# Performance work log

Hardware: AMD Instinct MI355X
Metric: run time of the kernel (lower is better)

## Reference

```python
import jax, jax.numpy as jnp
import numpy as np

N_NODES = 100000
N_EDGES = 3200000
IN_DIM, HID_DIM, OUT_DIM = 384, 128, 5


def gcn_conv(x, src, dst, W, b, num_nodes):
    # PyG GCNConv: add self-loops, symmetric normalization, linear, aggregate, bias
    h = x @ W  # [N, out]
    ones = jnp.ones(src.shape[0], dtype=h.dtype)
    deg = jax.ops.segment_sum(ones, dst, num_segments=num_nodes)  # includes self-loops
    dinv = jnp.where(deg > 0, jax.lax.rsqrt(deg), 0.0)
    norm = dinv[src] * dinv[dst]  # [E+N]
    msg = h[src] * norm[:, None]
    out = jax.ops.segment_sum(msg, dst, num_segments=num_nodes)
    return out + b


def setup_inputs() -> dict:
    key = jax.random.key(0)
    ks = jax.random.split(key, 8)
    x = jax.random.normal(ks[0], (N_NODES, IN_DIM), dtype=jnp.float32)
    edge_index = jax.random.randint(ks[1], (2, N_EDGES), 0, N_NODES, dtype=jnp.int64)
    # Glorot-ish init for GCN linear weights
    def glorot(k, fi, fo):
        s = jnp.sqrt(6.0 / (fi + fo))
        return jax.random.uniform(k, (fi, fo), jnp.float32, -s, s)
    W1 = glorot(ks[2], IN_DIM, HID_DIM)
    b1 = jnp.zeros((HID_DIM,), jnp.float32)
    W2 = glorot(ks[3], HID_DIM, HID_DIM)
    b2 = jnp.zeros((HID_DIM,), jnp.float32)
    W3 = glorot(ks[4], HID_DIM, OUT_DIM)
    b3 = jnp.zeros((OUT_DIM,), jnp.float32)
    return {"x": x, "edge_index": edge_index, "W1": W1, "b1": b1,
            "W2": W2, "b2": b2, "W3": W3, "b3": b3}


def reference(x, edge_index, W1, b1, W2, b2, W3, b3):
    num_nodes = x.shape[0]
    loops = jnp.arange(num_nodes, dtype=edge_index.dtype)
    src = jnp.concatenate([edge_index[0], loops])
    dst = jnp.concatenate([edge_index[1], loops])
    # layer 1: GCNConv + ReLU (dropout is identity at inference)
    h = jax.nn.relu(gcn_conv(x, src, dst, W1, b1, num_nodes))
    # layer 2
    h = jax.nn.relu(gcn_conv(h, src, dst, W2, b2, num_nodes))
    # final layer: logits, no activation
    return gcn_conv(h, src, dst, W3, b3, num_nodes)
```

## Files before the change

kernel.cpp:

```cpp
#include <hip/hip_runtime.h>

#define NN 100000
#define NE 3200000
#define SCAN_CHUNK 1024

#define BSH 8
#define BKT_NODES 256
#define NBKT ((NN + BKT_NODES - 1) / BKT_NODES)
#define BIN_BLOCKS 256
#define EPB ((NE + BIN_BLOCKS - 1) / BIN_BLOCKS)
#define GH (NBKT * BIN_BLOCKS)

typedef unsigned int uint;
typedef unsigned short ushort;
typedef __attribute__((ext_vector_type(8))) short short8;
typedef __attribute__((ext_vector_type(4))) float f32x4;

__device__ inline void gload16(const void* g, void* l) {
    __builtin_amdgcn_global_load_lds(
        (const __attribute__((address_space(1))) void*)g,
        (__attribute__((address_space(3))) void*)l, 16, 0, 0);
}

__device__ inline ushort bf16rne(float x) {
    uint u = __float_as_uint(x);
    u += 0x7FFFu + ((u >> 16) & 1u);
    return (ushort)(u >> 16);
}
__device__ inline void split2(float x, ushort& h, ushort& l) {
    h = bf16rne(x);
    float hf = __uint_as_float((uint)h << 16);
    l = bf16rne(x - hf);
}
__device__ inline uint bf16pair(float a, float b) {
    uint ua = __float_as_uint(a);
    uint ub = __float_as_uint(b);
    ua += 0x7FFFu + ((ua >> 16) & 1u);
    ub += 0x7FFFu + ((ub >> 16) & 1u);
    return (ua >> 16) | (ub & 0xFFFF0000u);
}
__device__ inline float bflo(uint u) { return __uint_as_float(u << 16); }
__device__ inline float bfhi(uint u) { return __uint_as_float(u & 0xFFFF0000u); }

__global__ __launch_bounds__(256) void hist_bkt(const int* __restrict__ dst,
                                                int* __restrict__ ghist) {
    __shared__ int h[NBKT];
    int t = threadIdx.x;
    for (int i = t; i < NBKT; i += 256) h[i] = 0;
    __syncthreads();
    int beg = blockIdx.x * EPB;
    int end = beg + EPB; if (end > NE) end = NE;
    for (int e = beg + t; e < end; e += 256)
        atomicAdd(&h[dst[e] >> BSH], 1);
    __syncthreads();
    for (int i = t; i < NBKT; i += 256)
        ghist[i * BIN_BLOCKS + blockIdx.x] = h[i];
}

__global__ __launch_bounds__(256) void scan_p1(const int* __restrict__ cnt,
                                               int* __restrict__ bsum, int N) {
    int t = threadIdx.x;
    int base = blockIdx.x * SCAN_CHUNK + t * 4;
    int s = 0;
#pragma unroll
    for (int q = 0; q < 4; q++) {
        int i = base + q;
        if (i < N) s += cnt[i];
    }
    __shared__ int red[4];
#pragma unroll
    for (int off = 32; off; off >>= 1) s += __shfl_down(s, off, 64);
    if ((t & 63) == 0) red[t >> 6] = s;
    __syncthreads();
    if (t == 0) bsum[blockIdx.x] = red[0] + red[1] + red[2] + red[3];
}

__global__ void scan_p2(int* __restrict__ bsum, int nb) {
    __shared__ int s[128];
    int t = threadIdx.x;
    int v = (t < nb) ? bsum[t] : 0;
    s[t] = v;
    __syncthreads();
    for (int off = 1; off < 128; off <<= 1) {
        int x = s[t];
        int add = (t >= off) ? s[t - off] : 0;
        __syncthreads();
        s[t] = x + add;
        __syncthreads();
    }
    if (t < nb) bsum[t] = s[t] - v;
}

__global__ __launch_bounds__(256) void scan_p3_plain(int* __restrict__ data,
                                                     const int* __restrict__ bsum, int N) {
    __shared__ int ts[256];
    int t = threadIdx.x;
    int base = blockIdx.x * SCAN_CHUNK + t * 4;
    int c[4];
    int s = 0;
#pragma unroll
    for (int q = 0; q < 4; q++) {
        int i = base + q;
        c[q] = (i < N) ? data[i] : 0;
        s += c[q];
    }
    ts[t] = s;
    __syncthreads();
    for (int off = 1; off < 256; off <<= 1) {
        int x = ts[t];
        int add = (t >= off) ? ts[t - off] : 0;
        __syncthreads();
        ts[t] = x + add;
        __syncthreads();
    }
    int run = bsum[blockIdx.x] + ts[t] - s;
#pragma unroll
    for (int q = 0; q < 4; q++) {
        int i = base + q;
        if (i < N) { data[i] = run; run += c[q]; }
    }
}

__global__ __launch_bounds__(256) void scan_p3_deg(const int* __restrict__ cnt,
                                                   const int* __restrict__ bsum,
                                                   int* __restrict__ rowptr,
                                                   float* __restrict__ dinv, int N) {
    __shared__ int ts[256];
    int t = threadIdx.x;
    int base = blockIdx.x * SCAN_CHUNK + t * 4;
    int c[4];
    int s = 0;
#pragma unroll
    for (int q = 0; q < 4; q++) {
        int i = base + q;
        c[q] = (i < N) ? cnt[i] : 0;
        s += c[q];
    }
    ts[t] = s;
    __syncthreads();
    for (int off = 1; off < 256; off <<= 1) {
        int x = ts[t];
        int add = (t >= off) ? ts[t - off] : 0;
        __syncthreads();
        ts[t] = x + add;
        __syncthreads();
    }
    int run = bsum[blockIdx.x] + ts[t] - s;
#pragma unroll
    for (int q = 0; q < 4; q++) {
        int i = base + q;
        if (i < N) {
            rowptr[i] = run;
            dinv[i] = 1.0f / sqrtf((float)(c[q] + 1));
            run += c[q];
        }
    }
    if (base < N && N <= base + 4) rowptr[N] = run;
}

__global__ __launch_bounds__(256) void bin_edges(const int* __restrict__ src,
                                                 const int* __restrict__ dst,
                                                 const int* __restrict__ ghist,
                                                 uint* __restrict__ binned) {
    __shared__ int cur[NBKT];
    int t = threadIdx.x;
    for (int i = t; i < NBKT; i += 256) cur[i] = ghist[i * BIN_BLOCKS + blockIdx.x];
    __syncthreads();
    int beg = blockIdx.x * EPB;
    int end = beg + EPB; if (end > NE) end = NE;
    for (int e = beg + t; e < end; e += 256) {
        int d = dst[e];
        int b = d >> BSH;
        int p = atomicAdd(&cur[b], 1);
        binned[p] = ((uint)src[e] << BSH) | (uint)(d & (BKT_NODES - 1));
    }
}

__global__ __launch_bounds__(256) void bucket_count(const uint* __restrict__ binned,
                                                    const int* __restrict__ ghist,
                                                    int* __restrict__ cnt) {
    __shared__ int c[BKT_NODES];
    int t = threadIdx.x;
    int bkt = blockIdx.x;
    for (int i = t; i < BKT_NODES; i += 256) c[i] = 0;
    __syncthreads();
    int beg = ghist[bkt * BIN_BLOCKS];
    int end = (bkt == NBKT - 1) ? NE : ghist[(bkt + 1) * BIN_BLOCKS];
    for (int j = beg + t; j < end; j += 256)
        atomicAdd(&c[binned[j] & (BKT_NODES - 1)], 1);
    __syncthreads();
    int base = bkt * BKT_NODES;
    int nb = NN - base; if (nb > BKT_NODES) nb = BKT_NODES;
    for (int i = t; i < nb; i += 256) cnt[base + i] = c[i];
}

__global__ __launch_bounds__(256) void csr_fill(const uint* __restrict__ binned,
                                                const int* __restrict__ ghist,
                                                const int* __restrict__ rowptr,
                                                int* __restrict__ col) {
    __shared__ int fill[BKT_NODES];
    int t = threadIdx.x;
    int bkt = blockIdx.x;
    for (int i = t; i < BKT_NODES; i += 256) fill[i] = 0;
    __syncthreads();
    int beg = ghist[bkt * BIN_BLOCKS];
    int end = (bkt == NBKT - 1) ? NE : ghist[(bkt + 1) * BIN_BLOCKS];
    int base = bkt * BKT_NODES;
    for (int j = beg + t; j < end; j += 256) {
        uint r = binned[j];
        int dl = r & (BKT_NODES - 1);
        int p = rowptr[base + dl] + atomicAdd(&fill[dl], 1);
        col[p] = (int)(r >> BSH);
    }
}

template <int K>
__global__ __launch_bounds__(256) void wsplit(const float* __restrict__ W,
                                              ushort* __restrict__ Wth,
                                              ushort* __restrict__ Wtl) {
    __shared__ float tile[32][128];
    int t = threadIdx.x;
    int kb = blockIdx.x;
    {
        int k = t >> 3, cq = t & 7;
#pragma unroll
        for (int q = 0; q < 4; q++) {
            float4 v = *(const float4*)&W[(size_t)(kb * 32 + k) * 128 + cq * 16 + q * 4];
            *(float4*)&tile[k][cq * 16 + q * 4] = v;
        }
    }
    __syncthreads();
    {
        int c = t >> 1, g = t & 1;
        ushort hs[16], ls[16];
#pragma unroll
        for (int i = 0; i < 16; i++) split2(tile[g * 16 + i][c], hs[i], ls[i]);
        uint h[8], lo[8];
#pragma unroll
        for (int i = 0; i < 8; i++) {
            h[i] = (uint)hs[2 * i] | ((uint)hs[2 * i + 1] << 16);
            lo[i] = (uint)ls[2 * i] | ((uint)ls[2 * i + 1] << 16);
        }
        size_t o = (size_t)c * K + kb * 32 + g * 16;
        *(uint4*)&Wth[o] = make_uint4(h[0], h[1], h[2], h[3]);
        *(uint4*)&Wth[o + 8] = make_uint4(h[4], h[5], h[6], h[7]);
        *(uint4*)&Wtl[o] = make_uint4(lo[0], lo[1], lo[2], lo[3]);
        *(uint4*)&Wtl[o + 8] = make_uint4(lo[4], lo[5], lo[6], lo[7]);
    }
}

template <int K>
__global__ __launch_bounds__(256) void mfma_gemm(const float* __restrict__ X,
                                                 const ushort* __restrict__ Wth,
                                                 const ushort* __restrict__ Wtl,
                                                 const float* __restrict__ dinv,
                                                 uint* __restrict__ Y, int M) {
    __shared__ char smem[32 * 1024];
    char* aHi = smem;
    char* aLo = smem + 8192;
    char* bHi = smem + 16384;
    char* bLo = smem + 24576;
    int tid = threadIdx.x;
    int w = tid >> 6, l = tid & 63;
    int rowBase = blockIdx.x * 128;

    f32x4 acc[2][8];
#pragma unroll
    for (int mf = 0; mf < 2; mf++)
#pragma unroll
        for (int n = 0; n < 8; n++) acc[mf][n] = (f32x4){0.f, 0.f, 0.f, 0.f};

    int sRow = tid >> 1, sKp = tid & 1;
    int gRow = rowBase + sRow;
    bool rowOK = gRow < M;
    size_t aBase = (size_t)(rowOK ? gRow : 0) * K + sKp * 16;

    float4 a0, a1, a2, a3;
    a0 = a1 = a2 = a3 = make_float4(0.f, 0.f, 0.f, 0.f);
    if (rowOK) {
        a0 = *(const float4*)&X[aBase];
        a1 = *(const float4*)&X[aBase + 4];
        a2 = *(const float4*)&X[aBase + 8];
        a3 = *(const float4*)&X[aBase + 12];
    }

    int fc = l & 15, fkg = l >> 4;

    for (int kt = 0; kt < K; kt += 32) {
#pragma unroll
        for (int i = 0; i < 2; i++) {
            int cb = (i * 4 + w) * 64;
            int c = cb + l;
            int colb = c >> 2, kg = c & 3;
            size_t go = (size_t)colb * K + kt + kg * 8;
            gload16(&Wth[go], bHi + cb * 16);
            gload16(&Wtl[go], bLo + cb * 16);
        }
        {
            float v[16] = {a0.x, a0.y, a0.z, a0.w, a1.x, a1.y, a1.z, a1.w,
                           a2.x, a2.y, a2.z, a2.w, a3.x, a3.y, a3.z, a3.w};
            uint hh[8], hl[8];
#pragma unroll
            for (int i = 0; i < 8; i++) {
                ushort h0, l0, h1, l1;
                split2(v[2 * i], h0, l0);
                split2(v[2 * i + 1], h1, l1);
                hh[i] = (uint)h0 | ((uint)h1 << 16);
                hl[i] = (uint)l0 | ((uint)l1 << 16);
            }
            int wa = (sRow * 4 + sKp * 2) * 16;
            *(uint4*)(aHi + wa) = make_uint4(hh[0], hh[1], hh[2], hh[3]);
            *(uint4*)(aHi + wa + 16) = make_uint4(hh[4], hh[5], hh[6], hh[7]);
            *(uint4*)(aLo + wa) = make_uint4(hl[0], hl[1], hl[2], hl[3]);
            *(uint4*)(aLo + wa + 16) = make_uint4(hl[4], hl[5], hl[6], hl[7]);
        }
        __syncthreads();

        if (kt + 32 < K && rowOK) {
            size_t nb = aBase + kt + 32;
            a0 = *(const float4*)&X[nb];
            a1 = *(const float4*)&X[nb + 4];
            a2 = *(const float4*)&X[nb + 8];
            a3 = *(const float4*)&X[nb + 12];
        }

#pragma unroll
        for (int mf = 0; mf < 2; mf++) {
            int aoff = (((2 * w + mf) * 16 + fc) * 4 + fkg) * 16;
            short8 ah = *(const short8*)(aHi + aoff);
            short8 al = *(const short8*)(aLo + aoff);
#pragma unroll
            for (int n = 0; n < 8; n++) {
                int boff = ((16 * n + fc) * 4 + fkg) * 16;
                short8 bh = *(const short8*)(bHi + boff);
                short8 bl = *(const short8*)(bLo + boff);
                acc[mf][n] = __builtin_amdgcn_mfma_f32_16x16x32_bf16(ah, bh, acc[mf][n], 0, 0, 0);
                acc[mf][n] = __builtin_amdgcn_mfma_f32_16x16x32_bf16(ah, bl, acc[mf][n], 0, 0, 0);
                acc[mf][n] = __builtin_amdgcn_mfma_f32_16x16x32_bf16(al, bh, acc[mf][n], 0, 0, 0);
            }
        }
        __syncthreads();
    }

#pragma unroll
    for (int mf = 0; mf < 2; mf++) {
        float dscale[4];
#pragma unroll
        for (int r = 0; r < 4; r++) {
            int row = rowBase + (2 * w + mf) * 16 + fkg * 4 + r;
            dscale[r] = (row < M) ? dinv[row] : 0.f;
        }
#pragma unroll
        for (int n = 0; n < 8; n++) {
#pragma unroll
            for (int r = 0; r < 4; r++) {
                float val = acc[mf][n][r] * dscale[r];
                float p = __shfl_xor(val, 1, 64);
                int row = rowBase + (2 * w + mf) * 16 + fkg * 4 + r;
                if (!(l & 1) && row < M)
                    Y[(size_t)row * 64 + 8 * n + (fc >> 1)] = bf16pair(val, p);
            }
        }
    }
}

__global__ void gemm_n5(const float* __restrict__ X, const float* __restrict__ W,
                        float* __restrict__ Y, int M) {
    int idx = blockIdx.x * 256 + threadIdx.x;
    int row = idx / 5, c = idx % 5;
    if (row >= M) return;
    float acc = 0.f;
#pragma unroll 8
    for (int k = 0; k < 128; k++) acc += X[row * 128 + k] * W[k * 5 + c];
    Y[row * 5 + c] = acc;
}

__global__ void pack5(const float* __restrict__ Y, const float* __restrict__ dinv,
                      uint4* __restrict__ hc, int N) {
    int node = blockIdx.x * 256 + threadIdx.x;
    if (node >= N) return;
    float di = dinv[node];
    float v0 = Y[node * 5 + 0] * di;
    float v1 = Y[node * 5 + 1] * di;
    float v2 = Y[node * 5 + 2] * di;
    float v3 = Y[node * 5 + 3] * di;
    float v4 = Y[node * 5 + 4] * di;
    hc[node] = make_uint4(bf16pair(v0, v1), bf16pair(v2, v3), bf16pair(v4, 0.f), 0u);
}

#define ACC8(v)                         \
    a0 += bflo(v.x); a1 += bfhi(v.x);   \
    a2 += bflo(v.y); a3 += bfhi(v.y);   \
    a4 += bflo(v.z); a5 += bfhi(v.z);   \
    a6 += bflo(v.w); a7 += bfhi(v.w);

__global__ __launch_bounds__(256) void agg128_v3(const uint4* __restrict__ hb4,
                                                 const int* __restrict__ rowptr,
                                                 const int* __restrict__ col,
                                                 const float* __restrict__ dinv,
                                                 const float* __restrict__ bias,
                                                 float* __restrict__ out, int N, int do_relu) {
    int wave = threadIdx.x >> 6;
    int lane = threadIdx.x & 63;
    int node = blockIdx.x * 4 + wave;
    if (node >= N) return;
    int g = lane >> 4;
    int q = lane & 15;
    int beg = rowptr[node], end = rowptr[node + 1];
    float a0 = 0.f, a1 = 0.f, a2 = 0.f, a3 = 0.f, a4 = 0.f, a5 = 0.f, a6 = 0.f, a7 = 0.f;

    int j = beg;
    for (; j + 16 <= end; j += 16) {
        int s0 = col[j + g];
        int s1 = col[j + 4 + g];
        int s2 = col[j + 8 + g];
        int s3 = col[j + 12 + g];
        uint4 v0 = hb4[(size_t)s0 * 16 + q];
        uint4 v1 = hb4[(size_t)s1 * 16 + q];
        uint4 v2 = hb4[(size_t)s2 * 16 + q];
        uint4 v3 = hb4[(size_t)s3 * 16 + q];
        ACC8(v0); ACC8(v1); ACC8(v2); ACC8(v3);
    }
    if (j + 8 <= end) {
        int s0 = col[j + g];
        int s1 = col[j + 4 + g];
        uint4 v0 = hb4[(size_t)s0 * 16 + q];
        uint4 v1 = hb4[(size_t)s1 * 16 + q];
        ACC8(v0); ACC8(v1);
        j += 8;
    }
    if (j < end) {
        int jj0 = j + g, jj1 = j + 4 + g;
        bool p0 = jj0 < end, p1 = jj1 < end;
        int s0 = p0 ? col[jj0] : node;
        int s1 = p1 ? col[jj1] : node;
        uint4 v0 = hb4[(size_t)s0 * 16 + q];
        uint4 v1 = hb4[(size_t)s1 * 16 + q];
        if (!p0) v0 = make_uint4(0u, 0u, 0u, 0u);
        if (!p1) v1 = make_uint4(0u, 0u, 0u, 0u);
        ACC8(v0); ACC8(v1);
    }
#pragma unroll
    for (int off = 16; off <= 32; off <<= 1) {
        a0 += __shfl_xor(a0, off, 64);
        a1 += __shfl_xor(a1, off, 64);
        a2 += __shfl_xor(a2, off, 64);
        a3 += __shfl_xor(a3, off, 64);
        a4 += __shfl_xor(a4, off, 64);
        a5 += __shfl_xor(a5, off, 64);
        a6 += __shfl_xor(a6, off, 64);
        a7 += __shfl_xor(a7, off, 64);
    }
    if (g == 0) {
        uint4 vs = hb4[(size_t)node * 16 + q];
        ACC8(vs);
        float di = dinv[node];
        const float4* bias4 = (const float4*)bias;
        float4 bb0 = bias4[q * 2], bb1 = bias4[q * 2 + 1];
        float o0 = a0 * di + bb0.x, o1 = a1 * di + bb0.y;
        float o2 = a2 * di + bb0.z, o3 = a3 * di + bb0.w;
        float o4 = a4 * di + bb1.x, o5 = a5 * di + bb1.y;
        float o6 = a6 * di + bb1.z, o7 = a7 * di + bb1.w;
        if (do_relu) {
            o0 = fmaxf(o0, 0.f); o1 = fmaxf(o1, 0.f);
            o2 = fmaxf(o2, 0.f); o3 = fmaxf(o3, 0.f);
            o4 = fmaxf(o4, 0.f); o5 = fmaxf(o5, 0.f);
            o6 = fmaxf(o6, 0.f); o7 = fmaxf(o7, 0.f);
        }
        float4* out4 = (float4*)out;
        out4[(size_t)node * 32 + q * 2] = make_float4(o0, o1, o2, o3);
        out4[(size_t)node * 32 + q * 2 + 1] = make_float4(o4, o5, o6, o7);
    }
}

__global__ void agg5_v2(const uint4* __restrict__ hc, const int* __restrict__ rowptr,
                        const int* __restrict__ col, const float* __restrict__ dinv,
                        const float* __restrict__ b3, float* __restrict__ out, int N) {
    int node = blockIdx.x * 256 + threadIdx.x;
    if (node >= N) return;
    float a0 = 0.f, a1 = 0.f, a2 = 0.f, a3 = 0.f, a4 = 0.f;
    int beg = rowptr[node], end = rowptr[node + 1];
#pragma unroll 2
    for (int j = beg; j < end; ++j) {
        uint4 v = hc[col[j]];
        a0 += bflo(v.x); a1 += bfhi(v.x);
        a2 += bflo(v.y); a3 += bfhi(v.y);
        a4 += bflo(v.z);
    }
    uint4 vs = hc[node];
    a0 += bflo(vs.x); a1 += bfhi(vs.x);
    a2 += bflo(vs.y); a3 += bfhi(vs.y);
    a4 += bflo(vs.z);
    float di = dinv[node];
    out[node * 5 + 0] = a0 * di + b3[0];
    out[node * 5 + 1] = a1 * di + b3[1];
    out[node * 5 + 2] = a2 * di + b3[2];
    out[node * 5 + 3] = a3 * di + b3[3];
    out[node * 5 + 4] = a4 * di + b3[4];
}

static inline size_t align512(size_t x) { return (x + 511) & ~(size_t)511; }

extern "C" void kernel_launch(void* const* d_in, const int* in_sizes, int n_in,
                              void* d_out, int out_size, void* d_ws, size_t ws_size,
                              hipStream_t stream) {
    const float* x  = (const float*)d_in[0];
    const int* ei   = (const int*)d_in[1];
    const float* W1 = (const float*)d_in[2];
    const float* b1 = (const float*)d_in[3];
    const float* W2 = (const float*)d_in[4];
    const float* b2 = (const float*)d_in[5];
    const float* W3 = (const float*)d_in[6];
    const float* b3 = (const float*)d_in[7];
    const int* src = ei;
    const int* dst = ei + NE;

    char* ws = (char*)d_ws;
    size_t off = 0;
    int* cnt = (int*)(ws + off);        off += align512((size_t)NN * 4);
    int* rowptr = (int*)(ws + off);     off += align512((size_t)(NN + 1) * 4);
    float* dinv = (float*)(ws + off);   off += align512((size_t)NN * 4);
    int* bsum = (int*)(ws + off);       off += align512((size_t)128 * 4);
    int* ghist = (int*)(ws + off);      off += align512((size_t)GH * 4);
    ushort* wt1h = (ushort*)(ws + off); off += align512((size_t)128 * 384 * 2);
    ushort* wt1l = (ushort*)(ws + off); off += align512((size_t)128 * 384 * 2);
    ushort* wt2h = (ushort*)(ws + off); off += align512((size_t)128 * 128 * 2);
    ushort* wt2l = (ushort*)(ws + off); off += align512((size_t)128 * 128 * 2);
    int* col = (int*)(ws + off);        off += align512((size_t)NE * 4);
    uint* hb = (uint*)(ws + off);       off += align512((size_t)NN * 64 * 4);
    float* bufF = (float*)(ws + off);   off += align512((size_t)NN * 128 * 4);
    float* bufC = (float*)(ws + off);   off += align512((size_t)NN * 5 * 4);
    uint4* hc = (uint4*)(ws + off);     off += align512((size_t)NN * 16);
    uint* binned = (uint*)bufF;
    (void)ws_size;

    wsplit<384><<<12, 256, 0, stream>>>(W1, wt1h, wt1l);
    wsplit<128><<<4, 256, 0, stream>>>(W2, wt2h, wt2l);

    hist_bkt<<<BIN_BLOCKS, 256, 0, stream>>>(dst, ghist);
    {
        int nb = (GH + SCAN_CHUNK - 1) / SCAN_CHUNK;
        scan_p1<<<nb, 256, 0, stream>>>(ghist, bsum, GH);
        scan_p2<<<1, 128, 0, stream>>>(bsum, nb);
        scan_p3_plain<<<nb, 256, 0, stream>>>(ghist, bsum, GH);
    }
    bin_edges<<<BIN_BLOCKS, 256, 0, stream>>>(src, dst, ghist, binned);
    bucket_count<<<NBKT, 256, 0, stream>>>(binned, ghist, cnt);
    {
        int nb = (NN + SCAN_CHUNK - 1) / SCAN_CHUNK;
        scan_p1<<<nb, 256, 0, stream>>>(cnt, bsum, NN);
        scan_p2<<<1, 128, 0, stream>>>(bsum, nb);
        scan_p3_deg<<<nb, 256, 0, stream>>>(cnt, bsum, rowptr, dinv, NN);
    }
    csr_fill<<<NBKT, 256, 0, stream>>>(binned, ghist, rowptr, col);

    int gemm_blocks = (NN + 127) / 128;
    mfma_gemm<384><<<gemm_blocks, 256, 0, stream>>>(x, wt1h, wt1l, dinv, hb, NN);
    agg128_v3<<<(NN + 3) / 4, 256, 0, stream>>>((const uint4*)hb, rowptr, col, dinv, b1, bufF, NN, 1);
    mfma_gemm<128><<<gemm_blocks, 256, 0, stream>>>(bufF, wt2h, wt2l, dinv, hb, NN);
    agg128_v3<<<(NN + 3) / 4, 256, 0, stream>>>((const uint4*)hb, rowptr, col, dinv, b2, bufF, NN, 1);
    gemm_n5<<<((NN * 5) + 255) / 256, 256, 0, stream>>>(bufF, W3, bufC, NN);
    pack5<<<(NN + 255) / 256, 256, 0, stream>>>(bufC, dinv, hc, NN);
    agg5_v2<<<(NN + 255) / 256, 256, 0, stream>>>(hc, rowptr, col, dinv, b3, (float*)d_out, NN);
}
```

Measured before the change: 495.9 us.

## Switch GEMMs and intermediates from split bf16 to fp16 with fewer MFMAs

```diff
diff --git a/kernel.cpp b/kernel.cpp
--- a/kernel.cpp
+++ b/kernel.cpp
@@ -1,4 +1,5 @@
 #include <hip/hip_runtime.h>
+#include <hip/hip_fp16.h>
 
 #define NN 100000
 #define NE 3200000
@@ -13,7 +14,7 @@
 
 typedef unsigned int uint;
 typedef unsigned short ushort;
-typedef __attribute__((ext_vector_type(8))) short short8;
+typedef __attribute__((ext_vector_type(8))) _Float16 half8;
 typedef __attribute__((ext_vector_type(4))) float f32x4;
 
 __device__ inline void gload16(const void* g, void* l) {
@@ -22,25 +23,17 @@
         (__attribute__((address_space(3))) void*)l, 16, 0, 0);
 }
 
-__device__ inline ushort bf16rne(float x) {
-    uint u = __float_as_uint(x);
-    u += 0x7FFFu + ((u >> 16) & 1u);
-    return (ushort)(u >> 16);
-}
-__device__ inline void split2(float x, ushort& h, ushort& l) {
-    h = bf16rne(x);
-    float hf = __uint_as_float((uint)h << 16);
-    l = bf16rne(x - hf);
-}
-__device__ inline uint bf16pair(float a, float b) {
-    uint ua = __float_as_uint(a);
-    uint ub = __float_as_uint(b);
-    ua += 0x7FFFu + ((ua >> 16) & 1u);
-    ub += 0x7FFFu + ((ub >> 16) & 1u);
-    return (ua >> 16) | (ub & 0xFFFF0000u);
-}
-__device__ inline float bflo(uint u) { return __uint_as_float(u << 16); }
-__device__ inline float bfhi(uint u) { return __uint_as_float(u & 0xFFFF0000u); }
+__device__ inline uint f2h_pair(float a, float b) {
+    return (uint)__half_as_ushort(__float2half(a)) |
+           ((uint)__half_as_ushort(__float2half(b)) << 16);
+}
+__device__ inline float h2f_lo(uint u) { return __half2float(__ushort_as_half((ushort)(u & 0xFFFFu))); }
+__device__ inline float h2f_hi(uint u) { return __half2float(__ushort_as_half((ushort)(u >> 16))); }
+__device__ inline void splitH(float x, ushort& h, ushort& l) {
+    __half hh = __float2half(x);
+    h = __half_as_ushort(hh);
+    l = __half_as_ushort(__float2half(x - __half2float(hh)));
+}
 
 __global__ __launch_bounds__(256) void hist_bkt(const int* __restrict__ dst,
                                                 int* __restrict__ ghist) {
@@ -234,7 +227,7 @@
         int c = t >> 1, g = t & 1;
         ushort hs[16], ls[16];
 #pragma unroll
-        for (int i = 0; i < 16; i++) split2(tile[g * 16 + i][c], hs[i], ls[i]);
+        for (int i = 0; i < 16; i++) splitH(tile[g * 16 + i][c], hs[i], ls[i]);
         uint h[8], lo[8];
 #pragma unroll
         for (int i = 0; i < 8; i++) {
@@ -250,16 +243,15 @@
 }
 
 template <int K>
-__global__ __launch_bounds__(256) void mfma_gemm(const float* __restrict__ X,
-                                                 const ushort* __restrict__ Wth,
-                                                 const ushort* __restrict__ Wtl,
-                                                 const float* __restrict__ dinv,
-                                                 uint* __restrict__ Y, int M) {
-    __shared__ char smem[32 * 1024];
-    char* aHi = smem;
-    char* aLo = smem + 8192;
-    char* bHi = smem + 16384;
-    char* bLo = smem + 24576;
+__global__ __launch_bounds__(256) void mfma_gemm_f32(const float* __restrict__ X,
+                                                     const ushort* __restrict__ Wth,
+                                                     const ushort* __restrict__ Wtl,
+                                                     const float* __restrict__ dinv,
+                                                     uint* __restrict__ Y, int M) {
+    __shared__ char smem[24 * 1024];
+    char* aP = smem;
+    char* bH = smem + 8192;
+    char* bL = smem + 16384;
     int tid = threadIdx.x;
     int w = tid >> 6, l = tid & 63;
     int rowBase = blockIdx.x * 128;
@@ -285,34 +277,27 @@
     }
 
     int fc = l & 15, fkg = l >> 4;
+    int aoff0 = fkg * 2048 + ((2 * w + 0) * 16 + fc) * 16;
+    int aoff1 = fkg * 2048 + ((2 * w + 1) * 16 + fc) * 16;
 
     for (int kt = 0; kt < K; kt += 32) {
 #pragma unroll
         for (int i = 0; i < 2; i++) {
             int cb = (i * 4 + w) * 64;
             int c = cb + l;
-            int colb = c >> 2, kg = c & 3;
+            int kg = c >> 7, colb = c & 127;
             size_t go = (size_t)colb * K + kt + kg * 8;
-            gload16(&Wth[go], bHi + cb * 16);
-            gload16(&Wtl[go], bLo + cb * 16);
+            gload16(&Wth[go], bH + cb * 16);
+            gload16(&Wtl[go], bL + cb * 16);
         }
         {
             float v[16] = {a0.x, a0.y, a0.z, a0.w, a1.x, a1.y, a1.z, a1.w,
                            a2.x, a2.y, a2.z, a2.w, a3.x, a3.y, a3.z, a3.w};
-            uint hh[8], hl[8];
-#pragma unroll
-            for (int i = 0; i < 8; i++) {
-                ushort h0, l0, h1, l1;
-                split2(v[2 * i], h0, l0);
-                split2(v[2 * i + 1], h1, l1);
-                hh[i] = (uint)h0 | ((uint)h1 << 16);
-                hl[i] = (uint)l0 | ((uint)l1 << 16);
-            }
-            int wa = (sRow * 4 + sKp * 2) * 16;
-            *(uint4*)(aHi + wa) = make_uint4(hh[0], hh[1], hh[2], hh[3]);
-            *(uint4*)(aHi + wa + 16) = make_uint4(hh[4], hh[5], hh[6], hh[7]);
-            *(uint4*)(aLo + wa) = make_uint4(hl[0], hl[1], hl[2], hl[3]);
-            *(uint4*)(aLo + wa + 16) = make_uint4(hl[4], hl[5], hl[6], hl[7]);
+            uint hh[8];
+#pragma unroll
+            for (int i = 0; i < 8; i++) hh[i] = f2h_pair(v[2 * i], v[2 * i + 1]);
+            *(uint4*)(aP + (2 * sKp) * 2048 + sRow * 16) = make_uint4(hh[0], hh[1], hh[2], hh[3]);
+            *(uint4*)(aP + (2 * sKp + 1) * 2048 + sRow * 16) = make_uint4(hh[4], hh[5], hh[6], hh[7]);
         }
         __syncthreads();
 
@@ -324,20 +309,17 @@
             a3 = *(const float4*)&X[nb + 12];
         }
 
-#pragma unroll
-        for (int mf = 0; mf < 2; mf++) {
-            int aoff = (((2 * w + mf) * 16 + fc) * 4 + fkg) * 16;
-            short8 ah = *(const short8*)(aHi + aoff);
-            short8 al = *(const short8*)(aLo + aoff);
-#pragma unroll
-            for (int n = 0; n < 8; n++) {
-                int boff = ((16 * n + fc) * 4 + fkg) * 16;
-                short8 bh = *(const short8*)(bHi + boff);
-                short8 bl = *(const short8*)(bLo + boff);
-                acc[mf][n] = __builtin_amdgcn_mfma_f32_16x16x32_bf16(ah, bh, acc[mf][n], 0, 0, 0);
-                acc[mf][n] = __builtin_amdgcn_mfma_f32_16x16x32_bf16(ah, bl, acc[mf][n], 0, 0, 0);
-                acc[mf][n] = __builtin_amdgcn_mfma_f32_16x16x32_bf16(al, bh, acc[mf][n], 0, 0, 0);
-            }
+        half8 av0 = *(const half8*)(aP + aoff0);
+        half8 av1 = *(const half8*)(aP + aoff1);
+#pragma unroll
+        for (int n = 0; n < 8; n++) {
+            int boff = fkg * 2048 + (16 * n + fc) * 16;
+            half8 bh = *(const half8*)(bH + boff);
+            half8 bl = *(const half8*)(bL + boff);
+            acc[0][n] = __builtin_amdgcn_mfma_f32_16x16x32_f16(av0, bh, acc[0][n], 0, 0, 0);
+            acc[0][n] = __builtin_amdgcn_mfma_f32_16x16x32_f16(av0, bl, acc[0][n], 0, 0, 0);
+            acc[1][n] = __builtin_amdgcn_mfma_f32_16x16x32_f16(av1, bh, acc[1][n], 0, 0, 0);
+            acc[1][n] = __builtin_amdgcn_mfma_f32_16x16x32_f16(av1, bl, acc[1][n], 0, 0, 0);
         }
         __syncthreads();
     }
@@ -358,21 +340,114 @@
                 float p = __shfl_xor(val, 1, 64);
                 int row = rowBase + (2 * w + mf) * 16 + fkg * 4 + r;
                 if (!(l & 1) && row < M)
-                    Y[(size_t)row * 64 + 8 * n + (fc >> 1)] = bf16pair(val, p);
+                    Y[(size_t)row * 64 + 8 * n + (fc >> 1)] = f2h_pair(val, p);
             }
         }
     }
 }
 
-__global__ void gemm_n5(const float* __restrict__ X, const float* __restrict__ W,
-                        float* __restrict__ Y, int M) {
-    int idx = blockIdx.x * 256 + threadIdx.x;
-    int row = idx / 5, c = idx % 5;
+__global__ __launch_bounds__(256) void mfma_gemm_f16(const ushort* __restrict__ Xh,
+                                                     const ushort* __restrict__ Wth,
+                                                     const ushort* __restrict__ Wtl,
+                                                     const float* __restrict__ dinv,
+                                                     uint* __restrict__ Y, int M) {
+    __shared__ char smem[24 * 1024];
+    char* aP = smem;
+    char* bH = smem + 8192;
+    char* bL = smem + 16384;
+    int tid = threadIdx.x;
+    int w = tid >> 6, l = tid & 63;
+    int rowBase = blockIdx.x * 128;
+
+    f32x4 acc[2][8];
+#pragma unroll
+    for (int mf = 0; mf < 2; mf++)
+#pragma unroll
+        for (int n = 0; n < 8; n++) acc[mf][n] = (f32x4){0.f, 0.f, 0.f, 0.f};
+
+    int fc = l & 15, fkg = l >> 4;
+    int aoff0 = fkg * 2048 + ((2 * w + 0) * 16 + fc) * 16;
+    int aoff1 = fkg * 2048 + ((2 * w + 1) * 16 + fc) * 16;
+
+    for (int kt = 0; kt < 128; kt += 32) {
+#pragma unroll
+        for (int i = 0; i < 2; i++) {
+            int cb = (i * 4 + w) * 64;
+            int c = cb + l;
+            int kg = c >> 7, idx = c & 127;
+            gload16(&Xh[(size_t)(rowBase + idx) * 128 + kt + kg * 8], aP + cb * 16);
+            gload16(&Wth[(size_t)idx * 128 + kt + kg * 8], bH + cb * 16);
+            gload16(&Wtl[(size_t)idx * 128 + kt + kg * 8], bL + cb * 16);
+        }
+        __syncthreads();
+        half8 av0 = *(const half8*)(aP + aoff0);
+        half8 av1 = *(const half8*)(aP + aoff1);
+#pragma unroll
+        for (int n = 0; n < 8; n++) {
+            int boff = fkg * 2048 + (16 * n + fc) * 16;
+            half8 bh = *(const half8*)(bH + boff);
+            half8 bl = *(const half8*)(bL + boff);
+            acc[0][n] = __builtin_amdgcn_mfma_f32_16x16x32_f16(av0, bh, acc[0][n], 0, 0, 0);
+            acc[0][n] = __builtin_amdgcn_mfma_f32_16x16x32_f16(av0, bl, acc[0][n], 0, 0, 0);
+            acc[1][n] = __builtin_amdgcn_mfma_f32_16x16x32_f16(av1, bh, acc[1][n], 0, 0, 0);
+            acc[1][n] = __builtin_amdgcn_mfma_f32_16x16x32_f16(av1, bl, acc[1][n], 0, 0, 0);
+        }
+        __syncthreads();
+    }
+
+#pragma unroll
+    for (int mf = 0; mf < 2; mf++) {
+        float dscale[4];
+#pragma unroll
+        for (int r = 0; r < 4; r++) {
+            int row = rowBase + (2 * w + mf) * 16 + fkg * 4 + r;
+            dscale[r] = (row < M) ? dinv[row] : 0.f;
+        }
+#pragma unroll
+        for (int n = 0; n < 8; n++) {
+#pragma unroll
+            for (int r = 0; r < 4; r++) {
+                float val = acc[mf][n][r] * dscale[r];
+                float p = __shfl_xor(val, 1, 64);
+                int row = rowBase + (2 * w + mf) * 16 + fkg * 4 + r;
+                if (!(l & 1) && row < M)
+                    Y[(size_t)row * 64 + 8 * n + (fc >> 1)] = f2h_pair(val, p);
+            }
+        }
+    }
+}
+
+__global__ __launch_bounds__(256) void gemm_n5h(const uint4* __restrict__ Xh,
+                                                const float* __restrict__ W,
+                                                float* __restrict__ Y, int M) {
+    __shared__ float wl[640];
+    int t = threadIdx.x;
+    for (int i = t; i < 640; i += 256) wl[i] = W[i];
+    __syncthreads();
+    int row = blockIdx.x * 256 + t;
     if (row >= M) return;
-    float acc = 0.f;
-#pragma unroll 8
-    for (int k = 0; k < 128; k++) acc += X[row * 128 + k] * W[k * 5 + c];
-    Y[row * 5 + c] = acc;
+    float acc0 = 0.f, acc1 = 0.f, acc2 = 0.f, acc3 = 0.f, acc4 = 0.f;
+#pragma unroll
+    for (int kq = 0; kq < 16; kq++) {
+        uint4 v = Xh[(size_t)row * 16 + kq];
+        uint uu[4] = {v.x, v.y, v.z, v.w};
+#pragma unroll
+        for (int e = 0; e < 4; e++) {
+            float x0 = h2f_lo(uu[e]);
+            float x1 = h2f_hi(uu[e]);
+            int k = kq * 8 + e * 2;
+            acc0 = fmaf(x0, wl[k * 5 + 0], acc0); acc0 = fmaf(x1, wl[k * 5 + 5], acc0);
+            acc1 = fmaf(x0, wl[k * 5 + 1], acc1); acc1 = fmaf(x1, wl[k * 5 + 6], acc1);
+            acc2 = fmaf(x0, wl[k * 5 + 2], acc2); acc2 = fmaf(x1, wl[k * 5 + 7], acc2);
+            acc3 = fmaf(x0, wl[k * 5 + 3], acc3); acc3 = fmaf(x1, wl[k * 5 + 8], acc3);
+            acc4 = fmaf(x0, wl[k * 5 + 4], acc4); acc4 = fmaf(x1, wl[k * 5 + 9], acc4);
+        }
+    }
+    Y[row * 5 + 0] = acc0;
+    Y[row * 5 + 1] = acc1;
+    Y[row * 5 + 2] = acc2;
+    Y[row * 5 + 3] = acc3;
+    Y[row * 5 + 4] = acc4;
 }
 
 __global__ void pack5(const float* __restrict__ Y, const float* __restrict__ dinv,
@@ -385,21 +460,21 @@
     float v2 = Y[node * 5 + 2] * di;
     float v3 = Y[node * 5 + 3] * di;
     float v4 = Y[node * 5 + 4] * di;
-    hc[node] = make_uint4(bf16pair(v0, v1), bf16pair(v2, v3), bf16pair(v4, 0.f), 0u);
-}
-
-#define ACC8(v)                         \
-    a0 += bflo(v.x); a1 += bfhi(v.x);   \
-    a2 += bflo(v.y); a3 += bfhi(v.y);   \
-    a4 += bflo(v.z); a5 += bfhi(v.z);   \
-    a6 += bflo(v.w); a7 += bfhi(v.w);
+    hc[node] = make_uint4(f2h_pair(v0, v1), f2h_pair(v2, v3), f2h_pair(v4, 0.f), 0u);
+}
+
+#define ACC8H(v)                              \
+    a0 += h2f_lo(v.x); a1 += h2f_hi(v.x);     \
+    a2 += h2f_lo(v.y); a3 += h2f_hi(v.y);     \
+    a4 += h2f_lo(v.z); a5 += h2f_hi(v.z);     \
+    a6 += h2f_lo(v.w); a7 += h2f_hi(v.w);
 
 __global__ __launch_bounds__(256) void agg128_v3(const uint4* __restrict__ hb4,
                                                  const int* __restrict__ rowptr,
                                                  const int* __restrict__ col,
                                                  const float* __restrict__ dinv,
                                                  const float* __restrict__ bias,
-                                                 float* __restrict__ out, int N, int do_relu) {
+                                                 uint4* __restrict__ out, int N, int do_relu) {
     int wave = threadIdx.x >> 6;
     int lane = threadIdx.x & 63;
     int node = blockIdx.x * 4 + wave;
@@ -419,14 +494,14 @@
         uint4 v1 = hb4[(size_t)s1 * 16 + q];
         uint4 v2 = hb4[(size_t)s2 * 16 + q];
         uint4 v3 = hb4[(size_t)s3 * 16 + q];
-        ACC8(v0); ACC8(v1); ACC8(v2); ACC8(v3);
+        ACC8H(v0); ACC8H(v1); ACC8H(v2); ACC8H(v3);
     }
     if (j + 8 <= end) {
         int s0 = col[j + g];
         int s1 = col[j + 4 + g];
         uint4 v0 = hb4[(size_t)s0 * 16 + q];
         uint4 v1 = hb4[(size_t)s1 * 16 + q];
-        ACC8(v0); ACC8(v1);
+        ACC8H(v0); ACC8H(v1);
         j += 8;
     }
     if (j < end) {
@@ -438,7 +513,7 @@
         uint4 v1 = hb4[(size_t)s1 * 16 + q];
         if (!p0) v0 = make_uint4(0u, 0u, 0u, 0u);
         if (!p1) v1 = make_uint4(0u, 0u, 0u, 0u);
-        ACC8(v0); ACC8(v1);
+        ACC8H(v0); ACC8H(v1);
     }
 #pragma unroll
     for (int off = 16; off <= 32; off <<= 1) {
@@ -453,7 +528,7 @@
     }
     if (g == 0) {
         uint4 vs = hb4[(size_t)node * 16 + q];
-        ACC8(vs);
+        ACC8H(vs);
         float di = dinv[node];
         const float4* bias4 = (const float4*)bias;
         float4 bb0 = bias4[q * 2], bb1 = bias4[q * 2 + 1];
@@ -467,9 +542,8 @@
             o4 = fmaxf(o4, 0.f); o5 = fmaxf(o5, 0.f);
             o6 = fmaxf(o6, 0.f); o7 = fmaxf(o7, 0.f);
         }
-        float4* out4 = (float4*)out;
-        out4[(size_t)node * 32 + q * 2] = make_float4(o0, o1, o2, o3);
-        out4[(size_t)node * 32 + q * 2 + 1] = make_float4(o4, o5, o6, o7);
+        out[(size_t)node * 16 + q] =
+            make_uint4(f2h_pair(o0, o1), f2h_pair(o2, o3), f2h_pair(o4, o5), f2h_pair(o6, o7));
     }
 }
 
@@ -483,14 +557,14 @@
 #pragma unroll 2
     for (int j = beg; j < end; ++j) {
         uint4 v = hc[col[j]];
-        a0 += bflo(v.x); a1 += bfhi(v.x);
-        a2 += bflo(v.y); a3 += bfhi(v.y);
-        a4 += bflo(v.z);
+        a0 += h2f_lo(v.x); a1 += h2f_hi(v.x);
+        a2 += h2f_lo(v.y); a3 += h2f_hi(v.y);
+        a4 += h2f_lo(v.z);
     }
     uint4 vs = hc[node];
-    a0 += bflo(vs.x); a1 += bfhi(vs.x);
-    a2 += bflo(vs.y); a3 += bfhi(vs.y);
-    a4 += bflo(vs.z);
+    a0 += h2f_lo(vs.x); a1 += h2f_hi(vs.x);
+    a2 += h2f_lo(vs.y); a3 += h2f_hi(vs.y);
+    a4 += h2f_lo(vs.z);
     float di = dinv[node];
     out[node * 5 + 0] = a0 * di + b3[0];
     out[node * 5 + 1] = a1 * di + b3[1];
@@ -528,7 +602,7 @@
     ushort* wt2l = (ushort*)(ws + off); off += align512((size_t)128 * 128 * 2);
     int* col = (int*)(ws + off);        off += align512((size_t)NE * 4);
     uint* hb = (uint*)(ws + off);       off += align512((size_t)NN * 64 * 4);
-    float* bufF = (float*)(ws + off);   off += align512((size_t)NN * 128 * 4);
+    char* bufF = (char*)(ws + off);     off += align512((size_t)NN * 128 * 4);
     float* bufC = (float*)(ws + off);   off += align512((size_t)NN * 5 * 4);
     uint4* hc = (uint4*)(ws + off);     off += align512((size_t)NN * 16);
     uint* binned = (uint*)bufF;
@@ -555,11 +629,13 @@
     csr_fill<<<NBKT, 256, 0, stream>>>(binned, ghist, rowptr, col);
 
     int gemm_blocks = (NN + 127) / 128;
-    mfma_gemm<384><<<gemm_blocks, 256, 0, stream>>>(x, wt1h, wt1l, dinv, hb, NN);
-    agg128_v3<<<(NN + 3) / 4, 256, 0, stream>>>((const uint4*)hb, rowptr, col, dinv, b1, bufF, NN, 1);
-    mfma_gemm<128><<<gemm_blocks, 256, 0, stream>>>(bufF, wt2h, wt2l, dinv, hb, NN);
-    agg128_v3<<<(NN + 3) / 4, 256, 0, stream>>>((const uint4*)hb, rowptr, col, dinv, b2, bufF, NN, 1);
-    gemm_n5<<<((NN * 5) + 255) / 256, 256, 0, stream>>>(bufF, W3, bufC, NN);
+    mfma_gemm_f32<384><<<gemm_blocks, 256, 0, stream>>>(x, wt1h, wt1l, dinv, hb, NN);
+    agg128_v3<<<(NN + 3) / 4, 256, 0, stream>>>((const uint4*)hb, rowptr, col, dinv, b1,
+                                                (uint4*)bufF, NN, 1);
+    mfma_gemm_f16<<<gemm_blocks, 256, 0, stream>>>((const ushort*)bufF, wt2h, wt2l, dinv, hb, NN);
+    agg128_v3<<<(NN + 3) / 4, 256, 0, stream>>>((const uint4*)hb, rowptr, col, dinv, b2,
+                                                (uint4*)bufF, NN, 1);
+    gemm_n5h<<<(NN + 255) / 256, 256, 0, stream>>>((const uint4*)bufF, W3, bufC, NN);
     pack5<<<(NN + 255) / 256, 256, 0, stream>>>(bufC, dinv, hc, NN);
     agg5_v2<<<(NN + 255) / 256, 256, 0, stream>>>(hc, rowptr, col, dinv, b3, (float*)d_out, NN);
 }
```

Result: faster. 427.8 us (-13.7%).
